# Optimization experiments

Hardware: AMD Instinct MI355X
Metric: run time of the kernel (lower is better)

Reference implementation:

```python
import jax, jax.numpy as jnp
import numpy as np

WINDOW = 4  # window_size
H = 8       # n_heads


def setup_inputs() -> dict:
    key = jax.random.key(0)
    ks = jax.random.split(key, 12)
    B, C, T = 4, 512, 1024
    d = C // H
    x = jax.random.normal(ks[0], (B, C, T), dtype=jnp.float32)
    mask = jnp.ones((B, 1, 1, T), dtype=jnp.int32)
    s = 0.02
    Wq = jax.random.normal(ks[1], (C, C), dtype=jnp.float32) * s
    Wk = jax.random.normal(ks[2], (C, C), dtype=jnp.float32) * s
    Wv = jax.random.normal(ks[3], (C, C), dtype=jnp.float32) * s
    Wo = jax.random.normal(ks[4], (C, C), dtype=jnp.float32) * s
    bq = jnp.zeros((C,), jnp.float32)
    bk = jnp.zeros((C,), jnp.float32)
    bv = jnp.zeros((C,), jnp.float32)
    bo = jnp.zeros((C,), jnp.float32)
    rel_std = d ** (-0.5)
    emb_rel_k = jax.random.normal(ks[5], (1, 2 * WINDOW + 1, d), dtype=jnp.float32) * rel_std
    emb_rel_v = jax.random.normal(ks[6], (1, 2 * WINDOW + 1, d), dtype=jnp.float32) * rel_std
    return {"x": x, "mask": mask, "Wq": Wq, "bq": bq, "Wk": Wk, "bk": bk,
            "Wv": Wv, "bv": bv, "Wo": Wo, "bo": bo,
            "emb_rel_k": emb_rel_k, "emb_rel_v": emb_rel_v}


def _slice_rel_emb(emb, T, pad_len, start, end):
    # F.pad(emb, [0,0,pad,pad,0,0]) then [:, start:end] -> [1, 2T-1, d]
    p = jnp.pad(emb, ((0, 0), (pad_len, pad_len), (0, 0)))
    return p[:, start:end]


def reference(x, mask, Wq, bq, Wk, bk, Wv, bv, Wo, bo, emb_rel_k, emb_rel_v):
    B, C, T = x.shape
    d = C // H
    scale = jnp.asarray(np.sqrt(d), x.dtype)

    def proj(Wm, bm):
        return jnp.einsum('oc,bct->bot', Wm, x) + bm[None, :, None]

    def to_heads(t):  # [B,C,T] -> [B,H,T,d]
        return t.reshape(B, H, d, T).transpose(0, 1, 3, 2)

    query = to_heads(proj(Wq, bq))
    key_ = to_heads(proj(Wk, bk))
    value = to_heads(proj(Wv, bv))

    score = jnp.einsum('bhtd,bhsd->bhts', query, key_) / scale

    pad_len = max(0, T - (WINDOW + 1))
    start = max(0, WINDOW + 1 - T)
    end = start + 2 * T - 1

    k_emb = _slice_rel_emb(emb_rel_k, T, pad_len, start, end)  # [1, 2T-1, d]
    rel = jnp.einsum('bhtd,rd->bhtr', query, k_emb[0])          # [B,H,T,2T-1]
    # skew trick: relative -> absolute
    rel = jnp.pad(rel, ((0, 0), (0, 0), (0, 0), (0, 1))).reshape(B, H, 2 * T * T)
    rel = jnp.pad(rel, ((0, 0), (0, 0), (0, T - 1))).reshape(B, H, T + 1, 2 * T - 1)
    score_loc = rel[:, :, :T, T - 1:] / scale
    score = score + score_loc

    score = jnp.where(mask == 0, jnp.asarray(-10000.0, score.dtype), score)
    p_attn = jax.nn.softmax(score, axis=-1)  # dropout=0 (eval)

    output = jnp.einsum('bhts,bhsd->bhtd', p_attn, value)

    # inverse skew: absolute -> relative weights [B,H,T,2T-1]
    pw = jnp.pad(p_attn, ((0, 0), (0, 0), (0, 0), (0, T - 1))).reshape(B, H, T * (2 * T - 1))
    pw = jnp.pad(pw, ((0, 0), (0, 0), (T, 0))).reshape(B, H, T, 2 * T)[:, :, :, 1:]
    v_emb = _slice_rel_emb(emb_rel_v, T, pad_len, start, end)  # [1, 2T-1, d]
    output = output + jnp.einsum('bhtr,rd->bhtd', pw, v_emb[0])

    out = output.transpose(0, 1, 3, 2).reshape(B, C, T)
    return jnp.einsum('oc,bct->bot', Wo, out) + bo[None, :, None]
```

## Files before the change

### kernel.cpp

```cpp
#include <hip/hip_runtime.h>

typedef unsigned short u16;
typedef unsigned int u32;
using f32x4 = __attribute__((ext_vector_type(4))) float;
using s16x8 = __attribute__((ext_vector_type(8))) short;
using u16x4 = __attribute__((ext_vector_type(4))) unsigned short;
using u16x8 = __attribute__((ext_vector_type(8))) unsigned short;

#define GLOAD_LDS16(g, s)                                     \
  __builtin_amdgcn_global_load_lds(                           \
      (const __attribute__((address_space(1))) void*)(g),     \
      (__attribute__((address_space(3))) void*)(s), 16, 0, 0)

namespace {

constexpr int T = 1024;
constexpr int C = 512;
constexpr float QSCALE = 0.125f * 1.4426950408889634f;
constexpr float MASKED = -14427.0f;
constexpr float DEFER_THR = 11.0f;

__device__ inline u16 f2bf(float f) {
  u32 u = __builtin_bit_cast(u32, f);
  u32 r = (u + 0x7fffu + ((u >> 16) & 1u)) >> 16;
  return (u16)r;
}
__device__ inline float bf2f(u16 v) {
  return __builtin_bit_cast(float, (u32)v << 16);
}
__device__ inline f32x4 mfma16(s16x8 a, s16x8 b, f32x4 c) {
  return __builtin_amdgcn_mfma_f32_16x16x32_bf16(a, b, c, 0, 0, 0);
}
__device__ inline u32 cvtpk(float lo, float hi) {
  u32 r;
  asm("v_cvt_pk_bf16_f32 %0, %1, %2" : "=v"(r) : "v"(lo), "v"(hi));
  return r;
}

__global__ __launch_bounds__(256) void convert_all(
    const float* __restrict__ x, const float* __restrict__ Wq,
    const float* __restrict__ Wk, const float* __restrict__ Wv,
    const float* __restrict__ Wo, u16* __restrict__ xb, u16* __restrict__ Wqb,
    u16* __restrict__ Wkb, u16* __restrict__ Wvb, u16* __restrict__ Wob) {
  const int tid = threadIdx.x;
  const int bid = blockIdx.x;
  const float* src;
  u16* dst;
  size_t off;
  if (bid < 2048) {
    src = x; dst = xb;
    off = ((size_t)bid * 256 + tid) * 4;
  } else {
    const int j = bid - 2048;
    const int w = j >> 8;
    src = w == 0 ? Wq : w == 1 ? Wk : w == 2 ? Wv : Wo;
    dst = w == 0 ? Wqb : w == 1 ? Wkb : w == 2 ? Wvb : Wob;
    off = (((size_t)(j & 255)) * 256 + tid) * 4;
  }
  const float4 v = *reinterpret_cast<const float4*>(src + off);
  u16x4 o;
  o[0] = f2bf(v.x); o[1] = f2bf(v.y); o[2] = f2bf(v.z); o[3] = f2bf(v.w);
  *reinterpret_cast<u16x4*>(dst + off) = o;
}

__global__ __launch_bounds__(256) void qkv_gemm(
    const u16* __restrict__ xb, const u16* __restrict__ Wqb,
    const u16* __restrict__ Wkb, const u16* __restrict__ Wvb,
    const float* __restrict__ bq, const float* __restrict__ bk,
    const float* __restrict__ bv, u16* __restrict__ qb, u16* __restrict__ kswz,
    u16* __restrict__ vswz) {
  __shared__ u16 Bs[2][128 * 32];
  __shared__ float sbias[64];
  const int tid = threadIdx.x;
  const int z = blockIdx.z;
  const int b = z / 3, wsel = z - 3 * b;
  const u16* W = wsel == 0 ? Wqb : wsel == 1 ? Wkb : Wvb;
  const float* bias = wsel == 0 ? bq : wsel == 1 ? bk : bv;
  const int o0 = blockIdx.y * 64;
  const int t0 = blockIdx.x * 128;
  if (tid < 16)
    *reinterpret_cast<float4*>(&sbias[tid * 4]) =
        *reinterpret_cast<const float4*>(&bias[o0 + tid * 4]);

  const int l = tid & 63, wid = tid >> 6;
  const int wm = wid >> 1, wn = wid & 1;
  const int lr = l & 15, lg = l >> 4;

  const int cpair = tid & 15, tgrp = tid >> 4;
  const u16* xrow =
      xb + ((size_t)(b * C) + 2 * cpair) * T + t0 + 8 * tgrp;

  const u16* Arow0 = W + (size_t)(o0 + 32 * wm + lr) * C + 8 * lg;
  const u16* Arow1 = Arow0 + 16 * C;

  f32x4 acc[2][4] = {};

  auto stage = [&](int kk, int buf) {
    const u16* p = xrow + (size_t)kk * 32 * T;
    const u16x8 v0 = *reinterpret_cast<const u16x8*>(p);
    const u16x8 v1 = *reinterpret_cast<const u16x8*>(p + T);
    char* base = (char*)&Bs[buf][0];
#pragma unroll
    for (int j = 0; j < 8; ++j) {
      const int t = 8 * tgrp + j;
      const u32 w2 = (u32)v0[j] | ((u32)v1[j] << 16);
      *(u32*)(base + ((t * 64 + 4 * cpair) ^ ((t & 3) << 4))) = w2;
    }
  };

  s16x8 a0 = *reinterpret_cast<const s16x8*>(Arow0);
  s16x8 a1 = *reinterpret_cast<const s16x8*>(Arow1);
  stage(0, 0);
  __syncthreads();

  for (int kk = 0; kk < 16; ++kk) {
    s16x8 an0, an1;
    if (kk < 15) {
      an0 = *reinterpret_cast<const s16x8*>(Arow0 + (kk + 1) * 32);
      an1 = *reinterpret_cast<const s16x8*>(Arow1 + (kk + 1) * 32);
      stage(kk + 1, (kk + 1) & 1);
    }
    const char* rb = (const char*)&Bs[kk & 1][0];
#pragma unroll
    for (int nf = 0; nf < 4; ++nf) {
      const int t = 64 * wn + 16 * nf + lr;
      const s16x8 bfrag = *reinterpret_cast<const s16x8*>(
          rb + ((t * 64 + 16 * lg) ^ ((t & 3) << 4)));
      acc[0][nf] = mfma16(a0, bfrag, acc[0][nf]);
      acc[1][nf] = mfma16(a1, bfrag, acc[1][nf]);
    }
    __syncthreads();
    if (kk < 15) { a0 = an0; a1 = an1; }
  }

  const int h = o0 >> 6;
  const size_t bh = (size_t)(b * 8 + h);
  if (wsel == 0) {
#pragma unroll
    for (int m = 0; m < 2; ++m) {
      const int ob = 32 * wm + 16 * m + 4 * lg;
#pragma unroll
      for (int nf = 0; nf < 4; ++nf) {
        const int t = t0 + 64 * wn + 16 * nf + lr;
        u16x4 pk;
#pragma unroll
        for (int r = 0; r < 4; ++r)
          pk[r] = f2bf((acc[m][nf][r] + sbias[ob + r]) * QSCALE);
        *reinterpret_cast<u16x4*>(&qb[(bh * T + t) * 64 + ob]) = pk;
      }
    }
  } else if (wsel == 1) {
    char* kbase = (char*)kswz;
#pragma unroll
    for (int m = 0; m < 2; ++m) {
      const int ob = 32 * wm + 16 * m + 4 * lg;
#pragma unroll
      for (int nf = 0; nf < 4; ++nf) {
        const int t = t0 + 64 * wn + 16 * nf + lr;
        const int tile = t >> 6, row = t & 63;
        u16x4 pk;
#pragma unroll
        for (int r = 0; r < 4; ++r) pk[r] = f2bf(acc[m][nf][r] + sbias[ob + r]);
        const int off = (row * 128 + 2 * ob) ^ ((row & 7) << 4);
        *(u16x4*)(kbase + (bh * 16 + tile) * 8192 + off) = pk;
      }
    }
  } else {
    char* vbase = (char*)vswz;
#pragma unroll
    for (int m = 0; m < 2; ++m) {
      const int ob = 32 * wm + 16 * m + 4 * lg;
#pragma unroll
      for (int nf = 0; nf < 4; ++nf) {
        const int t = t0 + 64 * wn + 16 * nf + lr;
        const int tile = t >> 6, col2 = 2 * (t & 63);
#pragma unroll
        for (int r = 0; r < 4; ++r) {
          const int dd = ob + r;
          const int off = (dd * 128 + col2) ^ ((dd & 7) << 4);
          *(u16*)(vbase + (bh * 16 + tile) * 8192 + off) =
              f2bf(acc[m][nf][r] + sbias[dd]);
        }
      }
    }
  }
}

__global__ __launch_bounds__(512) void attn_swapped(
    const u16* __restrict__ qb, const u16* __restrict__ kswz,
    const u16* __restrict__ vswz, const int* __restrict__ gmask,
    const float* __restrict__ ek, const float* __restrict__ ev,
    u16* __restrict__ op0, u16* __restrict__ op1, float2* __restrict__ mlb) {
  __shared__ u16 Kbuf[2][4096];
  __shared__ u16 Vbuf[2][4096];
  __shared__ char QsPd[16384];
  __shared__ float rkk[128][12];
  __shared__ float eks[9][64];
  __shared__ float evs[9][64];
  __shared__ u16 zerobuf[16];
  __shared__ int tflag[16];

  const int z = blockIdx.z;
  const int b = z >> 1, shalf = z & 1;
  const int h = blockIdx.y, tc = blockIdx.x * 128;
  const int tid = threadIdx.x;
  const int l = tid & 63, wid = tid >> 6;
  const int lr = l & 15, lg = l >> 4;

  const size_t bh = (size_t)(b * 8 + h);
  const u16* qrow = qb + (bh * T + tc) * 64;
  const u16* kimg0 = kswz + bh * 65536;
  const u16* vimg0 = vswz + bh * 65536;

  {
    char* qs = QsPd;
#pragma unroll
    for (int rep = 0; rep < 2; ++rep) {
      const int idx = rep * 512 + tid;
      const int t = idx >> 3, slot = idx & 7;
      const u16x8 v =
          *reinterpret_cast<const u16x8*>(&qrow[(size_t)t * 64 + 8 * slot]);
      *(u16x8*)(qs + ((t * 128 + 16 * slot) ^ ((t & 7) << 4))) = v;
    }
  }
  if (tid < 144) {
    reinterpret_cast<float4*>(&eks[0][0])[tid] =
        reinterpret_cast<const float4*>(ek)[tid];
    reinterpret_cast<float4*>(&evs[0][0])[tid] =
        reinterpret_cast<const float4*>(ev)[tid];
  }
  if (tid < 16) { tflag[tid] = 1; zerobuf[tid] = 0; }
  __syncthreads();

  if (tid < 256) {
    const int4 mm = reinterpret_cast<const int4*>(gmask + b * T)[tid];
    if (!(mm.x && mm.y && mm.z && mm.w)) tflag[tid >> 4] = 0;
  }

  auto stage_tile = [&](int st_abs, int buf) {
    const u16* ki = kimg0 + (size_t)st_abs * 4096;
    const u16* vi = vimg0 + (size_t)st_abs * 4096;
    GLOAD_LDS16(ki + wid * 512 + l * 8, &Kbuf[buf][wid * 512]);
    GLOAD_LDS16(vi + wid * 512 + l * 8, &Vbuf[buf][wid * 512]);
  };
  const int st0 = shalf * 8;
  stage_tile(st0, 0);

  {
    const char* qs = QsPd;
    for (int task = tid; task < 1152; task += 512) {
      const int r = task / 9, w = task - 9 * r;
      float s = 0.f;
      const float* er = &eks[w][0];
#pragma unroll 8
      for (int dd = 0; dd < 64; ++dd) {
        const u16 qv = *(const u16*)(qs + ((r * 128 + 2 * dd) ^ ((r & 7) << 4)));
        s += bf2f(qv) * er[dd];
      }
      rkk[r][w] = s;
    }
  }

  const int tA = 16 * wid + lr;
  s16x8 aq0, aq1;
  {
    const char* qs = QsPd;
    aq0 = *reinterpret_cast<const s16x8*>(
        qs + ((tA * 128 + 16 * lg) ^ ((tA & 7) << 4)));
    aq1 = *reinterpret_cast<const s16x8*>(
        qs + ((tA * 128 + 16 * (lg + 4)) ^ ((tA & 7) << 4)));
  }
  __syncthreads();

  u16* Pd = (u16*)(QsPd + wid * 512);

  s16x8 evA[4];
#pragma unroll
  for (int nf = 0; nf < 4; ++nf) {
    const int dd = 16 * nf + lr;
#pragma unroll
    for (int e = 0; e < 8; ++e) {
      float v = 0.f;
      if (lg == 0) v = evs[e][dd];
      else if (lg == 1 && e == 0) v = evs[8][dd];
      evA[nf][e] = (short)f2bf(v);
    }
  }

  float m = -1e30f, lsum = 0.f;
  f32x4 Oa[4] = {};
  const int tbw = tc + 16 * wid;
  const int qg = tbw + lr;

  int cur = 0;
  for (int i = 0; i < 8; ++i) {
    const int st = st0 + i;
    const int s0 = st * 64;
    if (i < 7) stage_tile(st + 1, cur ^ 1);

    f32x4 St[4] = {};
    const char* ksb = (const char*)&Kbuf[cur][0];
#pragma unroll
    for (int nf = 0; nf < 4; ++nf) {
      const int srow = 16 * nf + lr;
      const int swz = (srow & 7) << 4;
      const s16x8 bk0 = *reinterpret_cast<const s16x8*>(
          ksb + ((srow * 128 + 16 * lg) ^ swz));
      const s16x8 bk1 = *reinterpret_cast<const s16x8*>(
          ksb + ((srow * 128 + 16 * (lg + 4)) ^ swz));
      St[nf] = mfma16(bk0, aq0, St[nf]);
      St[nf] = mfma16(bk1, aq1, St[nf]);
    }

    const bool diagw = (s0 <= tbw + 19) && (s0 + 63 >= tbw - 4);

    if (diagw) {
#pragma unroll
      for (int nf = 0; nf < 4; ++nf)
#pragma unroll
        for (int r = 0; r < 4; ++r) {
          const int sd = (s0 + 16 * nf + 4 * lg + r) - qg;
          if (sd >= -4 && sd <= 4) St[nf][r] += rkk[16 * wid + lr][sd + 4];
        }
    }
    if (!tflag[st]) {
#pragma unroll
      for (int nf = 0; nf < 4; ++nf)
#pragma unroll
        for (int r = 0; r < 4; ++r) {
          if (gmask[b * T + s0 + 16 * nf + 4 * lg + r] == 0)
            St[nf][r] = MASKED;
        }
    }

    float rm;
    {
      float m0 = fmaxf(fmaxf(St[0][0], St[0][1]), fmaxf(St[0][2], St[0][3]));
      float m1 = fmaxf(fmaxf(St[1][0], St[1][1]), fmaxf(St[1][2], St[1][3]));
      float m2 = fmaxf(fmaxf(St[2][0], St[2][1]), fmaxf(St[2][2], St[2][3]));
      float m3 = fmaxf(fmaxf(St[3][0], St[3][1]), fmaxf(St[3][2], St[3][3]));
      rm = fmaxf(fmaxf(m0, m1), fmaxf(m2, m3));
      rm = fmaxf(rm, __shfl_xor(rm, 16));
      rm = fmaxf(rm, __shfl_xor(rm, 32));
    }
    if (!__all(rm - m <= DEFER_THR)) {
      const float mn = fmaxf(m, rm);
      const float corr = exp2f(m - mn);
#pragma unroll
      for (int nf = 0; nf < 4; ++nf) {
        Oa[nf][0] *= corr; Oa[nf][1] *= corr;
        Oa[nf][2] *= corr; Oa[nf][3] *= corr;
      }
      lsum *= corr;
      m = mn;
    }
    float rs = 0.f;
#pragma unroll
    for (int nf = 0; nf < 4; ++nf)
#pragma unroll
      for (int r = 0; r < 4; ++r) {
        const float p = exp2f(St[nf][r] - m);
        St[nf][r] = p;
        rs += p;
      }
    rs += __shfl_xor(rs, 16);
    rs += __shfl_xor(rs, 32);
    lsum += rs;

    u32 wpk[4][2];
#pragma unroll
    for (int nf = 0; nf < 4; ++nf) {
      wpk[nf][0] = cvtpk(St[nf][0], St[nf][1]);
      wpk[nf][1] = cvtpk(St[nf][2], St[nf][3]);
    }

    if (diagw) {
      u32* pz = (u32*)Pd;
      pz[l] = 0; pz[l + 64] = 0;
#pragma unroll
      for (int nf = 0; nf < 4; ++nf)
#pragma unroll
        for (int r = 0; r < 4; ++r) {
          const int sd = (s0 + 16 * nf + 4 * lg + r) - qg;
          if (sd >= -4 && sd <= 4) Pd[lr * 16 + sd + 4] = f2bf(St[nf][r]);
        }
    }

    const int srcLo = lr + ((lg & 1) << 5);
    const int srcHi = srcLo + 16;
    const bool hiSel = (lg >> 1) != 0;
    union { u32 u[4]; s16x8 v; } pa0, pa1;
    {
      const u32 a0_ = __shfl((int)wpk[0][0], srcLo), b0_ = __shfl((int)wpk[1][0], srcLo);
      const u32 a1_ = __shfl((int)wpk[0][1], srcLo), b1_ = __shfl((int)wpk[1][1], srcLo);
      const u32 a2_ = __shfl((int)wpk[0][0], srcHi), b2_ = __shfl((int)wpk[1][0], srcHi);
      const u32 a3_ = __shfl((int)wpk[0][1], srcHi), b3_ = __shfl((int)wpk[1][1], srcHi);
      pa0.u[0] = hiSel ? b0_ : a0_; pa0.u[1] = hiSel ? b1_ : a1_;
      pa0.u[2] = hiSel ? b2_ : a2_; pa0.u[3] = hiSel ? b3_ : a3_;
    }
    {
      const u32 a0_ = __shfl((int)wpk[2][0], srcLo), b0_ = __shfl((int)wpk[3][0], srcLo);
      const u32 a1_ = __shfl((int)wpk[2][1], srcLo), b1_ = __shfl((int)wpk[3][1], srcLo);
      const u32 a2_ = __shfl((int)wpk[2][0], srcHi), b2_ = __shfl((int)wpk[3][0], srcHi);
      const u32 a3_ = __shfl((int)wpk[2][1], srcHi), b3_ = __shfl((int)wpk[3][1], srcHi);
      pa1.u[0] = hiSel ? b0_ : a0_; pa1.u[1] = hiSel ? b1_ : a1_;
      pa1.u[2] = hiSel ? b2_ : a2_; pa1.u[3] = hiSel ? b3_ : a3_;
    }

    const char* vsb = (const char*)&Vbuf[cur][0];
#pragma unroll
    for (int nf = 0; nf < 4; ++nf) {
      const int dd = 16 * nf + lr;
      const int swz = (dd & 7) << 4;
      const s16x8 bv0 = *reinterpret_cast<const s16x8*>(
          vsb + ((dd * 128 + 16 * lg) ^ swz));
      const s16x8 bv1 = *reinterpret_cast<const s16x8*>(
          vsb + ((dd * 128 + 16 * (lg + 4)) ^ swz));
      Oa[nf] = mfma16(bv0, pa0.v, Oa[nf]);
      Oa[nf] = mfma16(bv1, pa1.v, Oa[nf]);
    }

    if (diagw) {
      const u16* pdsrc = (lg < 2) ? &Pd[lr * 16 + 8 * lg] : &zerobuf[0];
      const s16x8 pd = *reinterpret_cast<const s16x8*>(pdsrc);
#pragma unroll
      for (int nf = 0; nf < 4; ++nf) Oa[nf] = mfma16(evA[nf], pd, Oa[nf]);
    }

    __syncthreads();
    cur ^= 1;
  }

  u16* op = shalf ? op1 : op0;
#pragma unroll
  for (int nf = 0; nf < 4; ++nf) {
    u16x4 pk;
#pragma unroll
    for (int r = 0; r < 4; ++r) pk[r] = f2bf(Oa[nf][r]);
    *reinterpret_cast<u16x4*>(
        &op[(bh * T + qg) * 64 + 16 * nf + 4 * lg]) = pk;
  }
  if (lg == 0) {
    float2 v;
    v.x = m;
    v.y = lsum;
    mlb[(size_t)shalf * 32768 + bh * T + qg] = v;
  }
}

__global__ __launch_bounds__(256) void merge_halves(
    const u16* __restrict__ op0, const u16* __restrict__ op1,
    const float2* __restrict__ mlb, u16* __restrict__ attb) {
  const int tid = threadIdx.x;
  const int row = blockIdx.x * 16 + (tid >> 4);
  const int dd = (tid & 15) * 4;
  const float2 ml0 = mlb[row];
  const float2 ml1 = mlb[32768 + row];
  const float mm = fmaxf(ml0.x, ml1.x);
  const float a0 = exp2f(ml0.x - mm), a1 = exp2f(ml1.x - mm);
  const float inv = 1.0f / (a0 * ml0.y + a1 * ml1.y);
  const u16x4 v0 = *reinterpret_cast<const u16x4*>(&op0[(size_t)row * 64 + dd]);
  const u16x4 v1 = *reinterpret_cast<const u16x4*>(&op1[(size_t)row * 64 + dd]);
  u16x4 o;
#pragma unroll
  for (int j = 0; j < 4; ++j)
    o[j] = f2bf((bf2f(v0[j]) * a0 + bf2f(v1[j]) * a1) * inv);
  *reinterpret_cast<u16x4*>(&attb[(size_t)row * 64 + dd]) = o;
}

__global__ __launch_bounds__(256) void out_gemm(
    const u16* __restrict__ Wob, const float* __restrict__ bo,
    const u16* __restrict__ attb, float* __restrict__ out) {
  __shared__ u16 Bs[2][128 * 32];
  __shared__ float sbias[64];
  const int tid = threadIdx.x;
  const int b = blockIdx.z;
  const int o0 = blockIdx.y * 64;
  const int t0 = blockIdx.x * 128;
  if (tid < 16)
    *reinterpret_cast<float4*>(&sbias[tid * 4]) =
        *reinterpret_cast<const float4*>(&bo[o0 + tid * 4]);

  const int l = tid & 63, wid = tid >> 6;
  const int wm = wid >> 1, wn = wid & 1;
  const int lr = l & 15, lg = l >> 4;

  const int slot = tid & 3, trow = tid >> 2;
  const u16* Arow0 = Wob + (size_t)(o0 + 32 * wm + lr) * C + 8 * lg;
  const u16* Arow1 = Arow0 + 16 * C;

  f32x4 acc[2][4] = {};

  auto stage = [&](int kk, int buf) {
    const int c0 = kk * 32;
    const int h = c0 >> 6, dd0 = c0 & 63;
    char* base = (char*)&Bs[buf][0];
#pragma unroll
    for (int rep = 0; rep < 2; ++rep) {
      const int t = rep * 64 + trow;
      const u16x8 v = *reinterpret_cast<const u16x8*>(
          &attb[((size_t)((b * 8 + h) * T) + t0 + t) * 64 + dd0 + 8 * slot]);
      *(u16x8*)(base + ((t * 64 + 16 * slot) ^ ((t & 3) << 4))) = v;
    }
  };

  s16x8 a0 = *reinterpret_cast<const s16x8*>(Arow0);
  s16x8 a1 = *reinterpret_cast<const s16x8*>(Arow1);
  stage(0, 0);
  __syncthreads();

  for (int kk = 0; kk < 16; ++kk) {
    s16x8 an0, an1;
    if (kk < 15) {
      an0 = *reinterpret_cast<const s16x8*>(Arow0 + (kk + 1) * 32);
      an1 = *reinterpret_cast<const s16x8*>(Arow1 + (kk + 1) * 32);
      stage(kk + 1, (kk + 1) & 1);
    }
    const char* rb = (const char*)&Bs[kk & 1][0];
#pragma unroll
    for (int nf = 0; nf < 4; ++nf) {
      const int t = 64 * wn + 16 * nf + lr;
      const s16x8 bfrag = *reinterpret_cast<const s16x8*>(
          rb + ((t * 64 + 16 * lg) ^ ((t & 3) << 4)));
      acc[0][nf] = mfma16(a0, bfrag, acc[0][nf]);
      acc[1][nf] = mfma16(a1, bfrag, acc[1][nf]);
    }
    __syncthreads();
    if (kk < 15) { a0 = an0; a1 = an1; }
  }

#pragma unroll
  for (int m = 0; m < 2; ++m) {
    const int ol = 32 * wm + 16 * m + 4 * lg;
#pragma unroll
    for (int nf = 0; nf < 4; ++nf) {
      const int t = t0 + 64 * wn + 16 * nf + lr;
#pragma unroll
      for (int r = 0; r < 4; ++r)
        out[((size_t)(b * C) + o0 + ol + r) * T + t] =
            acc[m][nf][r] + sbias[ol + r];
    }
  }
}

}

extern "C" void kernel_launch(void* const* d_in, const int* in_sizes, int n_in,
                              void* d_out, int out_size, void* d_ws,
                              size_t ws_size, hipStream_t stream) {
  const float* x    = (const float*)d_in[0];
  const int*   mask = (const int*)d_in[1];
  const float* Wq   = (const float*)d_in[2];
  const float* bq   = (const float*)d_in[3];
  const float* Wk   = (const float*)d_in[4];
  const float* bk   = (const float*)d_in[5];
  const float* Wv   = (const float*)d_in[6];
  const float* bv   = (const float*)d_in[7];
  const float* Wo   = (const float*)d_in[8];
  const float* bo   = (const float*)d_in[9];
  const float* ek   = (const float*)d_in[10];
  const float* ev   = (const float*)d_in[11];
  float* out = (float*)d_out;

  char* ws = (char*)d_ws;
  u16* xb   = (u16*)(ws);
  u16* Wqb  = (u16*)(ws + 4194304);
  u16* Wkb  = (u16*)(ws + 4718592);
  u16* Wvb  = (u16*)(ws + 5242880);
  u16* Wob  = (u16*)(ws + 5767168);
  u16* qb   = (u16*)(ws + 6291456);
  u16* kswz = (u16*)(ws + 10485760);
  u16* vswz = (u16*)(ws + 14680064);
  u16* attb = (u16*)(ws + 18874368);
  u16* op0  = xb;
  u16* op1  = (u16*)(ws + 23068672);
  float2* mlb = (float2*)(ws + 27262976);

  convert_all<<<dim3(3072), dim3(256), 0, stream>>>(x, Wq, Wk, Wv, Wo, xb, Wqb,
                                                    Wkb, Wvb, Wob);
  qkv_gemm<<<dim3(8, 8, 12), dim3(256), 0, stream>>>(xb, Wqb, Wkb, Wvb, bq, bk,
                                                     bv, qb, kswz, vswz);
  attn_swapped<<<dim3(8, 8, 8), dim3(512), 0, stream>>>(
      qb, kswz, vswz, mask, ek, ev, op0, op1, mlb);
  merge_halves<<<dim3(2048), dim3(256), 0, stream>>>(op0, op1, mlb, attb);
  out_gemm<<<dim3(8, 8, 4), dim3(256), 0, stream>>>(Wob, bo, attb, out);
}
```

Baseline: 89.11 us.

## Fuse bf16 conversion into GEMMs and split attention keys into thirds

Drops the separate convert_all kernel: both the QKV and output GEMMs now load fp32 x and weights directly and pack them to bf16 in registers with v_cvt_pk_bf16_f32. The attention kernel splits the key range into three chunks instead of two, which raises the block count, and a three-way merge kernel combines them. It also loads Q fragments straight from global memory and computes the relative-key dot products with a 4-lane shuffle reduction, which frees the Q staging buffer in LDS. In exchange the GEMMs read twice the bytes per operand and convert the same data again in every block that uses it, and the merge reads one more partial buffer.

```diff
diff --git a/kernel.cpp b/kernel.cpp
--- a/kernel.cpp
+++ b/kernel.cpp
@@ -36,36 +36,20 @@
   asm("v_cvt_pk_bf16_f32 %0, %1, %2" : "=v"(r) : "v"(lo), "v"(hi));
   return r;
 }
-
-__global__ __launch_bounds__(256) void convert_all(
+__device__ inline s16x8 ldfrag_f32(const float* p) {
+  const float4 f0 = *reinterpret_cast<const float4*>(p);
+  const float4 f1 = *reinterpret_cast<const float4*>(p + 4);
+  union { u32 u[4]; s16x8 v; } r;
+  r.u[0] = cvtpk(f0.x, f0.y);
+  r.u[1] = cvtpk(f0.z, f0.w);
+  r.u[2] = cvtpk(f1.x, f1.y);
+  r.u[3] = cvtpk(f1.z, f1.w);
+  return r.v;
+}
+
+__global__ __launch_bounds__(256) void qkv_gemm(
     const float* __restrict__ x, const float* __restrict__ Wq,
     const float* __restrict__ Wk, const float* __restrict__ Wv,
-    const float* __restrict__ Wo, u16* __restrict__ xb, u16* __restrict__ Wqb,
-    u16* __restrict__ Wkb, u16* __restrict__ Wvb, u16* __restrict__ Wob) {
-  const int tid = threadIdx.x;
-  const int bid = blockIdx.x;
-  const float* src;
-  u16* dst;
-  size_t off;
-  if (bid < 2048) {
-    src = x; dst = xb;
-    off = ((size_t)bid * 256 + tid) * 4;
-  } else {
-    const int j = bid - 2048;
-    const int w = j >> 8;
-    src = w == 0 ? Wq : w == 1 ? Wk : w == 2 ? Wv : Wo;
-    dst = w == 0 ? Wqb : w == 1 ? Wkb : w == 2 ? Wvb : Wob;
-    off = (((size_t)(j & 255)) * 256 + tid) * 4;
-  }
-  const float4 v = *reinterpret_cast<const float4*>(src + off);
-  u16x4 o;
-  o[0] = f2bf(v.x); o[1] = f2bf(v.y); o[2] = f2bf(v.z); o[3] = f2bf(v.w);
-  *reinterpret_cast<u16x4*>(dst + off) = o;
-}
-
-__global__ __launch_bounds__(256) void qkv_gemm(
-    const u16* __restrict__ xb, const u16* __restrict__ Wqb,
-    const u16* __restrict__ Wkb, const u16* __restrict__ Wvb,
     const float* __restrict__ bq, const float* __restrict__ bk,
     const float* __restrict__ bv, u16* __restrict__ qb, u16* __restrict__ kswz,
     u16* __restrict__ vswz) {
@@ -74,7 +58,7 @@
   const int tid = threadIdx.x;
   const int z = blockIdx.z;
   const int b = z / 3, wsel = z - 3 * b;
-  const u16* W = wsel == 0 ? Wqb : wsel == 1 ? Wkb : Wvb;
+  const float* W = wsel == 0 ? Wq : wsel == 1 ? Wk : Wv;
   const float* bias = wsel == 0 ? bq : wsel == 1 ? bk : bv;
   const int o0 = blockIdx.y * 64;
   const int t0 = blockIdx.x * 128;
@@ -87,37 +71,40 @@
   const int lr = l & 15, lg = l >> 4;
 
   const int cpair = tid & 15, tgrp = tid >> 4;
-  const u16* xrow =
-      xb + ((size_t)(b * C) + 2 * cpair) * T + t0 + 8 * tgrp;
-
-  const u16* Arow0 = W + (size_t)(o0 + 32 * wm + lr) * C + 8 * lg;
-  const u16* Arow1 = Arow0 + 16 * C;
+  const float* xrow = x + ((size_t)(b * C) + 2 * cpair) * T + t0 + 8 * tgrp;
+
+  const float* Arow0 = W + (size_t)(o0 + 32 * wm + lr) * C + 8 * lg;
+  const float* Arow1 = Arow0 + 16 * C;
 
   f32x4 acc[2][4] = {};
 
   auto stage = [&](int kk, int buf) {
-    const u16* p = xrow + (size_t)kk * 32 * T;
-    const u16x8 v0 = *reinterpret_cast<const u16x8*>(p);
-    const u16x8 v1 = *reinterpret_cast<const u16x8*>(p + T);
+    const float* p = xrow + (size_t)kk * 32 * T;
+    const float4 e0 = *reinterpret_cast<const float4*>(p);
+    const float4 e1 = *reinterpret_cast<const float4*>(p + 4);
+    const float4 o0_ = *reinterpret_cast<const float4*>(p + T);
+    const float4 o1_ = *reinterpret_cast<const float4*>(p + T + 4);
+    const float ev_[8] = {e0.x, e0.y, e0.z, e0.w, e1.x, e1.y, e1.z, e1.w};
+    const float od_[8] = {o0_.x, o0_.y, o0_.z, o0_.w, o1_.x, o1_.y, o1_.z, o1_.w};
     char* base = (char*)&Bs[buf][0];
 #pragma unroll
     for (int j = 0; j < 8; ++j) {
       const int t = 8 * tgrp + j;
-      const u32 w2 = (u32)v0[j] | ((u32)v1[j] << 16);
+      const u32 w2 = cvtpk(ev_[j], od_[j]);
       *(u32*)(base + ((t * 64 + 4 * cpair) ^ ((t & 3) << 4))) = w2;
     }
   };
 
-  s16x8 a0 = *reinterpret_cast<const s16x8*>(Arow0);
-  s16x8 a1 = *reinterpret_cast<const s16x8*>(Arow1);
+  s16x8 a0 = ldfrag_f32(Arow0);
+  s16x8 a1 = ldfrag_f32(Arow1);
   stage(0, 0);
   __syncthreads();
 
   for (int kk = 0; kk < 16; ++kk) {
     s16x8 an0, an1;
     if (kk < 15) {
-      an0 = *reinterpret_cast<const s16x8*>(Arow0 + (kk + 1) * 32);
-      an1 = *reinterpret_cast<const s16x8*>(Arow1 + (kk + 1) * 32);
+      an0 = ldfrag_f32(Arow0 + (kk + 1) * 32);
+      an1 = ldfrag_f32(Arow1 + (kk + 1) * 32);
       stage(kk + 1, (kk + 1) & 1);
     }
     const char* rb = (const char*)&Bs[kk & 1][0];
@@ -190,10 +177,11 @@
     const u16* __restrict__ qb, const u16* __restrict__ kswz,
     const u16* __restrict__ vswz, const int* __restrict__ gmask,
     const float* __restrict__ ek, const float* __restrict__ ev,
-    u16* __restrict__ op0, u16* __restrict__ op1, float2* __restrict__ mlb) {
+    u16* __restrict__ op0, u16* __restrict__ op1, u16* __restrict__ op2,
+    float2* __restrict__ mlb) {
   __shared__ u16 Kbuf[2][4096];
   __shared__ u16 Vbuf[2][4096];
-  __shared__ char QsPd[16384];
+  __shared__ u16 Pdiag[8][256];
   __shared__ float rkk[128][12];
   __shared__ float eks[9][64];
   __shared__ float evs[9][64];
@@ -201,28 +189,19 @@
   __shared__ int tflag[16];
 
   const int z = blockIdx.z;
-  const int b = z >> 1, shalf = z & 1;
+  const int b = z / 3, third = z - 3 * b;
   const int h = blockIdx.y, tc = blockIdx.x * 128;
   const int tid = threadIdx.x;
   const int l = tid & 63, wid = tid >> 6;
   const int lr = l & 15, lg = l >> 4;
+  const int stS = (third == 0) ? 0 : (third == 1) ? 6 : 11;
+  const int stE = (third == 0) ? 6 : (third == 1) ? 11 : 16;
 
   const size_t bh = (size_t)(b * 8 + h);
-  const u16* qrow = qb + (bh * T + tc) * 64;
+  const u16* qbh = qb + bh * T * 64;
   const u16* kimg0 = kswz + bh * 65536;
   const u16* vimg0 = vswz + bh * 65536;
 
-  {
-    char* qs = QsPd;
-#pragma unroll
-    for (int rep = 0; rep < 2; ++rep) {
-      const int idx = rep * 512 + tid;
-      const int t = idx >> 3, slot = idx & 7;
-      const u16x8 v =
-          *reinterpret_cast<const u16x8*>(&qrow[(size_t)t * 64 + 8 * slot]);
-      *(u16x8*)(qs + ((t * 128 + 16 * slot) ^ ((t & 7) << 4))) = v;
-    }
-  }
   if (tid < 144) {
     reinterpret_cast<float4*>(&eks[0][0])[tid] =
         reinterpret_cast<const float4*>(ek)[tid];
@@ -231,11 +210,6 @@
   }
   if (tid < 16) { tflag[tid] = 1; zerobuf[tid] = 0; }
   __syncthreads();
-
-  if (tid < 256) {
-    const int4 mm = reinterpret_cast<const int4*>(gmask + b * T)[tid];
-    if (!(mm.x && mm.y && mm.z && mm.w)) tflag[tid >> 4] = 0;
-  }
 
   auto stage_tile = [&](int st_abs, int buf) {
     const u16* ki = kimg0 + (size_t)st_abs * 4096;
@@ -243,36 +217,52 @@
     GLOAD_LDS16(ki + wid * 512 + l * 8, &Kbuf[buf][wid * 512]);
     GLOAD_LDS16(vi + wid * 512 + l * 8, &Vbuf[buf][wid * 512]);
   };
-  const int st0 = shalf * 8;
-  stage_tile(st0, 0);
+  stage_tile(stS, 0);
+
+  if (tid < 256) {
+    const int4 mm = reinterpret_cast<const int4*>(gmask + b * T)[tid];
+    if (!(mm.x && mm.y && mm.z && mm.w)) tflag[tid >> 4] = 0;
+  }
 
   {
-    const char* qs = QsPd;
-    for (int task = tid; task < 1152; task += 512) {
-      const int r = task / 9, w = task - 9 * r;
+    const int r = tid >> 2, sub = tid & 3;
+    const u16* qp = qbh + (size_t)(tc + r) * 64 + sub * 16;
+    const u16x8 q0 = *reinterpret_cast<const u16x8*>(qp);
+    const u16x8 q1 = *reinterpret_cast<const u16x8*>(qp + 8);
+    float qf[16];
+#pragma unroll
+    for (int j = 0; j < 8; ++j) {
+      qf[j] = bf2f(q0[j]);
+      qf[j + 8] = bf2f(q1[j]);
+    }
+    float part[9];
+#pragma unroll
+    for (int w = 0; w < 9; ++w) {
       float s = 0.f;
-      const float* er = &eks[w][0];
-#pragma unroll 8
-      for (int dd = 0; dd < 64; ++dd) {
-        const u16 qv = *(const u16*)(qs + ((r * 128 + 2 * dd) ^ ((r & 7) << 4)));
-        s += bf2f(qv) * er[dd];
-      }
-      rkk[r][w] = s;
-    }
-  }
-
-  const int tA = 16 * wid + lr;
+      const float* er = &eks[w][sub * 16];
+#pragma unroll
+      for (int d = 0; d < 16; ++d) s += qf[d] * er[d];
+      part[w] = s;
+    }
+#pragma unroll
+    for (int w = 0; w < 9; ++w) {
+      part[w] += __shfl_xor(part[w], 1);
+      part[w] += __shfl_xor(part[w], 2);
+    }
+    if (sub == 0) {
+#pragma unroll
+      for (int w = 0; w < 9; ++w) rkk[r][w] = part[w];
+    }
+  }
+
+  const int tbw = tc + 16 * wid;
+  const int qg = tbw + lr;
   s16x8 aq0, aq1;
   {
-    const char* qs = QsPd;
-    aq0 = *reinterpret_cast<const s16x8*>(
-        qs + ((tA * 128 + 16 * lg) ^ ((tA & 7) << 4)));
-    aq1 = *reinterpret_cast<const s16x8*>(
-        qs + ((tA * 128 + 16 * (lg + 4)) ^ ((tA & 7) << 4)));
-  }
-  __syncthreads();
-
-  u16* Pd = (u16*)(QsPd + wid * 512);
+    const u16* qgp = qbh + (size_t)qg * 64;
+    aq0 = *reinterpret_cast<const s16x8*>(qgp + 8 * lg);
+    aq1 = *reinterpret_cast<const s16x8*>(qgp + 32 + 8 * lg);
+  }
 
   s16x8 evA[4];
 #pragma unroll
@@ -289,14 +279,14 @@
 
   float m = -1e30f, lsum = 0.f;
   f32x4 Oa[4] = {};
-  const int tbw = tc + 16 * wid;
-  const int qg = tbw + lr;
+  u16* Pd = &Pdiag[wid][0];
+
+  __syncthreads();
 
   int cur = 0;
-  for (int i = 0; i < 8; ++i) {
-    const int st = st0 + i;
+  for (int st = stS; st < stE; ++st) {
     const int s0 = st * 64;
-    if (i < 7) stage_tile(st + 1, cur ^ 1);
+    if (st + 1 < stE) stage_tile(st + 1, cur ^ 1);
 
     f32x4 St[4] = {};
     const char* ksb = (const char*)&Kbuf[cur][0];
@@ -431,7 +421,7 @@
     cur ^= 1;
   }
 
-  u16* op = shalf ? op1 : op0;
+  u16* op = (third == 0) ? op0 : (third == 1) ? op1 : op2;
 #pragma unroll
   for (int nf = 0; nf < 4; ++nf) {
     u16x4 pk;
@@ -444,32 +434,36 @@
     float2 v;
     v.x = m;
     v.y = lsum;
-    mlb[(size_t)shalf * 32768 + bh * T + qg] = v;
-  }
-}
-
-__global__ __launch_bounds__(256) void merge_halves(
+    mlb[(size_t)third * 32768 + bh * T + qg] = v;
+  }
+}
+
+__global__ __launch_bounds__(256) void merge_thirds(
     const u16* __restrict__ op0, const u16* __restrict__ op1,
-    const float2* __restrict__ mlb, u16* __restrict__ attb) {
+    const u16* __restrict__ op2, const float2* __restrict__ mlb,
+    u16* __restrict__ attb) {
   const int tid = threadIdx.x;
   const int row = blockIdx.x * 16 + (tid >> 4);
   const int dd = (tid & 15) * 4;
   const float2 ml0 = mlb[row];
   const float2 ml1 = mlb[32768 + row];
-  const float mm = fmaxf(ml0.x, ml1.x);
-  const float a0 = exp2f(ml0.x - mm), a1 = exp2f(ml1.x - mm);
-  const float inv = 1.0f / (a0 * ml0.y + a1 * ml1.y);
+  const float2 ml2 = mlb[65536 + row];
+  const float mm = fmaxf(fmaxf(ml0.x, ml1.x), ml2.x);
+  const float a0 = exp2f(ml0.x - mm), a1 = exp2f(ml1.x - mm),
+              a2 = exp2f(ml2.x - mm);
+  const float inv = 1.0f / (a0 * ml0.y + a1 * ml1.y + a2 * ml2.y);
   const u16x4 v0 = *reinterpret_cast<const u16x4*>(&op0[(size_t)row * 64 + dd]);
   const u16x4 v1 = *reinterpret_cast<const u16x4*>(&op1[(size_t)row * 64 + dd]);
+  const u16x4 v2 = *reinterpret_cast<const u16x4*>(&op2[(size_t)row * 64 + dd]);
   u16x4 o;
 #pragma unroll
   for (int j = 0; j < 4; ++j)
-    o[j] = f2bf((bf2f(v0[j]) * a0 + bf2f(v1[j]) * a1) * inv);
+    o[j] = f2bf((bf2f(v0[j]) * a0 + bf2f(v1[j]) * a1 + bf2f(v2[j]) * a2) * inv);
   *reinterpret_cast<u16x4*>(&attb[(size_t)row * 64 + dd]) = o;
 }
 
 __global__ __launch_bounds__(256) void out_gemm(
-    const u16* __restrict__ Wob, const float* __restrict__ bo,
+    const float* __restrict__ Wo, const float* __restrict__ bo,
     const u16* __restrict__ attb, float* __restrict__ out) {
   __shared__ u16 Bs[2][128 * 32];
   __shared__ float sbias[64];
@@ -486,8 +480,8 @@
   const int lr = l & 15, lg = l >> 4;
 
   const int slot = tid & 3, trow = tid >> 2;
-  const u16* Arow0 = Wob + (size_t)(o0 + 32 * wm + lr) * C + 8 * lg;
-  const u16* Arow1 = Arow0 + 16 * C;
+  const float* Arow0 = Wo + (size_t)(o0 + 32 * wm + lr) * C + 8 * lg;
+  const float* Arow1 = Arow0 + 16 * C;
 
   f32x4 acc[2][4] = {};
 
@@ -504,16 +498,16 @@
     }
   };
 
-  s16x8 a0 = *reinterpret_cast<const s16x8*>(Arow0);
-  s16x8 a1 = *reinterpret_cast<const s16x8*>(Arow1);
+  s16x8 a0 = ldfrag_f32(Arow0);
+  s16x8 a1 = ldfrag_f32(Arow1);
   stage(0, 0);
   __syncthreads();
 
   for (int kk = 0; kk < 16; ++kk) {
     s16x8 an0, an1;
     if (kk < 15) {
-      an0 = *reinterpret_cast<const s16x8*>(Arow0 + (kk + 1) * 32);
-      an1 = *reinterpret_cast<const s16x8*>(Arow1 + (kk + 1) * 32);
+      an0 = ldfrag_f32(Arow0 + (kk + 1) * 32);
+      an1 = ldfrag_f32(Arow1 + (kk + 1) * 32);
       stage(kk + 1, (kk + 1) & 1);
     }
     const char* rb = (const char*)&Bs[kk & 1][0];
@@ -563,25 +557,19 @@
   float* out = (float*)d_out;
 
   char* ws = (char*)d_ws;
-  u16* xb   = (u16*)(ws);
-  u16* Wqb  = (u16*)(ws + 4194304);
-  u16* Wkb  = (u16*)(ws + 4718592);
-  u16* Wvb  = (u16*)(ws + 5242880);
-  u16* Wob  = (u16*)(ws + 5767168);
-  u16* qb   = (u16*)(ws + 6291456);
-  u16* kswz = (u16*)(ws + 10485760);
-  u16* vswz = (u16*)(ws + 14680064);
-  u16* attb = (u16*)(ws + 18874368);
-  u16* op0  = xb;
-  u16* op1  = (u16*)(ws + 23068672);
-  float2* mlb = (float2*)(ws + 27262976);
-
-  convert_all<<<dim3(3072), dim3(256), 0, stream>>>(x, Wq, Wk, Wv, Wo, xb, Wqb,
-                                                    Wkb, Wvb, Wob);
-  qkv_gemm<<<dim3(8, 8, 12), dim3(256), 0, stream>>>(xb, Wqb, Wkb, Wvb, bq, bk,
-                                                     bv, qb, kswz, vswz);
-  attn_swapped<<<dim3(8, 8, 8), dim3(512), 0, stream>>>(
-      qb, kswz, vswz, mask, ek, ev, op0, op1, mlb);
-  merge_halves<<<dim3(2048), dim3(256), 0, stream>>>(op0, op1, mlb, attb);
-  out_gemm<<<dim3(8, 8, 4), dim3(256), 0, stream>>>(Wob, bo, attb, out);
-}
+  u16* qb   = (u16*)(ws);
+  u16* kswz = (u16*)(ws + 4194304);
+  u16* vswz = (u16*)(ws + 8388608);
+  u16* op0  = (u16*)(ws + 12582912);
+  u16* op1  = (u16*)(ws + 16777216);
+  u16* op2  = (u16*)(ws + 20971520);
+  float2* mlb = (float2*)(ws + 25165824);
+  u16* attb = op0;
+
+  qkv_gemm<<<dim3(8, 8, 12), dim3(256), 0, stream>>>(x, Wq, Wk, Wv, bq, bk, bv,
+                                                     qb, kswz, vswz);
+  attn_swapped<<<dim3(8, 8, 12), dim3(512), 0, stream>>>(
+      qb, kswz, vswz, mask, ek, ev, op0, op1, op2, mlb);
+  merge_thirds<<<dim3(2048), dim3(256), 0, stream>>>(op0, op1, op2, mlb, attb);
+  out_gemm<<<dim3(8, 8, 4), dim3(256), 0, stream>>>(Wo, bo, attb, out);
+}
```

After: 113.1 us. 27.0% more time.

## Process two key tiles per iteration and load Q fragments directly from global

Applied to the files above, without the earlier changes.

The attention loop now stages and consumes pairs of 64-key K/V tiles per iteration, halving the number of barriers and loop trips while interleaving independent MFMA chains for the two score tiles. Q is no longer staged through shared memory: MFMA fragments are read straight from global, and the relative-key bias dot products are computed by four lanes per row with shuffle reductions. The costs are doubled K/V LDS buffers and more live registers, which may lower occupancy.

```diff
diff --git a/kernel.cpp b/kernel.cpp
--- a/kernel.cpp
+++ b/kernel.cpp
@@ -191,9 +191,9 @@
     const u16* __restrict__ vswz, const int* __restrict__ gmask,
     const float* __restrict__ ek, const float* __restrict__ ev,
     u16* __restrict__ op0, u16* __restrict__ op1, float2* __restrict__ mlb) {
-  __shared__ u16 Kbuf[2][4096];
-  __shared__ u16 Vbuf[2][4096];
-  __shared__ char QsPd[16384];
+  __shared__ u16 Kbuf[2][8192];
+  __shared__ u16 Vbuf[2][8192];
+  __shared__ u16 Pdiag[8][256];
   __shared__ float rkk[128][12];
   __shared__ float eks[9][64];
   __shared__ float evs[9][64];
@@ -208,21 +208,10 @@
   const int lr = l & 15, lg = l >> 4;
 
   const size_t bh = (size_t)(b * 8 + h);
-  const u16* qrow = qb + (bh * T + tc) * 64;
+  const u16* qbh = qb + bh * T * 64;
   const u16* kimg0 = kswz + bh * 65536;
   const u16* vimg0 = vswz + bh * 65536;
 
-  {
-    char* qs = QsPd;
-#pragma unroll
-    for (int rep = 0; rep < 2; ++rep) {
-      const int idx = rep * 512 + tid;
-      const int t = idx >> 3, slot = idx & 7;
-      const u16x8 v =
-          *reinterpret_cast<const u16x8*>(&qrow[(size_t)t * 64 + 8 * slot]);
-      *(u16x8*)(qs + ((t * 128 + 16 * slot) ^ ((t & 7) << 4))) = v;
-    }
-  }
   if (tid < 144) {
     reinterpret_cast<float4*>(&eks[0][0])[tid] =
         reinterpret_cast<const float4*>(ek)[tid];
@@ -232,47 +221,63 @@
   if (tid < 16) { tflag[tid] = 1; zerobuf[tid] = 0; }
   __syncthreads();
 
+  auto stage_pair = [&](int stp, int buf) {
+    const u16* ki = kimg0 + (size_t)stp * 4096;
+    const u16* vi = vimg0 + (size_t)stp * 4096;
+#pragma unroll
+    for (int j = 0; j < 2; ++j) {
+      const int seg = wid + 8 * j;
+      GLOAD_LDS16(ki + seg * 512 + l * 8, &Kbuf[buf][seg * 512]);
+      GLOAD_LDS16(vi + seg * 512 + l * 8, &Vbuf[buf][seg * 512]);
+    }
+  };
+  const int st0 = shalf * 8;
+  stage_pair(st0, 0);
+
   if (tid < 256) {
     const int4 mm = reinterpret_cast<const int4*>(gmask + b * T)[tid];
     if (!(mm.x && mm.y && mm.z && mm.w)) tflag[tid >> 4] = 0;
   }
 
-  auto stage_tile = [&](int st_abs, int buf) {
-    const u16* ki = kimg0 + (size_t)st_abs * 4096;
-    const u16* vi = vimg0 + (size_t)st_abs * 4096;
-    GLOAD_LDS16(ki + wid * 512 + l * 8, &Kbuf[buf][wid * 512]);
-    GLOAD_LDS16(vi + wid * 512 + l * 8, &Vbuf[buf][wid * 512]);
-  };
-  const int st0 = shalf * 8;
-  stage_tile(st0, 0);
-
   {
-    const char* qs = QsPd;
-    for (int task = tid; task < 1152; task += 512) {
-      const int r = task / 9, w = task - 9 * r;
+    const int r = tid >> 2, sub = tid & 3;
+    const u16* qp = qbh + (size_t)(tc + r) * 64 + sub * 16;
+    const u16x8 q0 = *reinterpret_cast<const u16x8*>(qp);
+    const u16x8 q1 = *reinterpret_cast<const u16x8*>(qp + 8);
+    float qf[16];
+#pragma unroll
+    for (int j = 0; j < 8; ++j) {
+      qf[j] = bf2f(q0[j]);
+      qf[j + 8] = bf2f(q1[j]);
+    }
+    float part[9];
+#pragma unroll
+    for (int w = 0; w < 9; ++w) {
       float s = 0.f;
-      const float* er = &eks[w][0];
-#pragma unroll 8
-      for (int dd = 0; dd < 64; ++dd) {
-        const u16 qv = *(const u16*)(qs + ((r * 128 + 2 * dd) ^ ((r & 7) << 4)));
-        s += bf2f(qv) * er[dd];
-      }
-      rkk[r][w] = s;
-    }
-  }
-
-  const int tA = 16 * wid + lr;
+      const float* er = &eks[w][sub * 16];
+#pragma unroll
+      for (int d = 0; d < 16; ++d) s += qf[d] * er[d];
+      part[w] = s;
+    }
+#pragma unroll
+    for (int w = 0; w < 9; ++w) {
+      part[w] += __shfl_xor(part[w], 1);
+      part[w] += __shfl_xor(part[w], 2);
+    }
+    if (sub == 0) {
+#pragma unroll
+      for (int w = 0; w < 9; ++w) rkk[r][w] = part[w];
+    }
+  }
+
+  const int tbw = tc + 16 * wid;
+  const int qg = tbw + lr;
   s16x8 aq0, aq1;
   {
-    const char* qs = QsPd;
-    aq0 = *reinterpret_cast<const s16x8*>(
-        qs + ((tA * 128 + 16 * lg) ^ ((tA & 7) << 4)));
-    aq1 = *reinterpret_cast<const s16x8*>(
-        qs + ((tA * 128 + 16 * (lg + 4)) ^ ((tA & 7) << 4)));
-  }
-  __syncthreads();
-
-  u16* Pd = (u16*)(QsPd + wid * 512);
+    const u16* qgp = qbh + (size_t)qg * 64;
+    aq0 = *reinterpret_cast<const s16x8*>(qgp + 8 * lg);
+    aq1 = *reinterpret_cast<const s16x8*>(qgp + 32 + 8 * lg);
+  }
 
   s16x8 evA[4];
 #pragma unroll
@@ -289,103 +294,17 @@
 
   float m = -1e30f, lsum = 0.f;
   f32x4 Oa[4] = {};
-  const int tbw = tc + 16 * wid;
-  const int qg = tbw + lr;
-
-  int cur = 0;
-  for (int i = 0; i < 8; ++i) {
-    const int st = st0 + i;
-    const int s0 = st * 64;
-    if (i < 7) stage_tile(st + 1, cur ^ 1);
-
-    f32x4 St[4] = {};
-    const char* ksb = (const char*)&Kbuf[cur][0];
-#pragma unroll
-    for (int nf = 0; nf < 4; ++nf) {
-      const int srow = 16 * nf + lr;
-      const int swz = (srow & 7) << 4;
-      const s16x8 bk0 = *reinterpret_cast<const s16x8*>(
-          ksb + ((srow * 128 + 16 * lg) ^ swz));
-      const s16x8 bk1 = *reinterpret_cast<const s16x8*>(
-          ksb + ((srow * 128 + 16 * (lg + 4)) ^ swz));
-      St[nf] = mfma16(bk0, aq0, St[nf]);
-      St[nf] = mfma16(bk1, aq1, St[nf]);
-    }
-
-    const bool diagw = (s0 <= tbw + 19) && (s0 + 63 >= tbw - 4);
-
-    if (diagw) {
-#pragma unroll
-      for (int nf = 0; nf < 4; ++nf)
-#pragma unroll
-        for (int r = 0; r < 4; ++r) {
-          const int sd = (s0 + 16 * nf + 4 * lg + r) - qg;
-          if (sd >= -4 && sd <= 4) St[nf][r] += rkk[16 * wid + lr][sd + 4];
-        }
-    }
-    if (!tflag[st]) {
-#pragma unroll
-      for (int nf = 0; nf < 4; ++nf)
-#pragma unroll
-        for (int r = 0; r < 4; ++r) {
-          if (gmask[b * T + s0 + 16 * nf + 4 * lg + r] == 0)
-            St[nf][r] = MASKED;
-        }
-    }
-
-    float rm;
-    {
-      float m0 = fmaxf(fmaxf(St[0][0], St[0][1]), fmaxf(St[0][2], St[0][3]));
-      float m1 = fmaxf(fmaxf(St[1][0], St[1][1]), fmaxf(St[1][2], St[1][3]));
-      float m2 = fmaxf(fmaxf(St[2][0], St[2][1]), fmaxf(St[2][2], St[2][3]));
-      float m3 = fmaxf(fmaxf(St[3][0], St[3][1]), fmaxf(St[3][2], St[3][3]));
-      rm = fmaxf(fmaxf(m0, m1), fmaxf(m2, m3));
-      rm = fmaxf(rm, __shfl_xor(rm, 16));
-      rm = fmaxf(rm, __shfl_xor(rm, 32));
-    }
-    if (!__all(rm - m <= DEFER_THR)) {
-      const float mn = fmaxf(m, rm);
-      const float corr = exp2f(m - mn);
-#pragma unroll
-      for (int nf = 0; nf < 4; ++nf) {
-        Oa[nf][0] *= corr; Oa[nf][1] *= corr;
-        Oa[nf][2] *= corr; Oa[nf][3] *= corr;
-      }
-      lsum *= corr;
-      m = mn;
-    }
-    float rs = 0.f;
-#pragma unroll
-    for (int nf = 0; nf < 4; ++nf)
-#pragma unroll
-      for (int r = 0; r < 4; ++r) {
-        const float p = exp2f(St[nf][r] - m);
-        St[nf][r] = p;
-        rs += p;
-      }
-    rs += __shfl_xor(rs, 16);
-    rs += __shfl_xor(rs, 32);
-    lsum += rs;
-
+  u16* Pd = &Pdiag[wid][0];
+
+  __syncthreads();
+
+  auto redist = [&](const f32x4* St, s16x8& pv0, s16x8& pv1) {
     u32 wpk[4][2];
 #pragma unroll
     for (int nf = 0; nf < 4; ++nf) {
       wpk[nf][0] = cvtpk(St[nf][0], St[nf][1]);
       wpk[nf][1] = cvtpk(St[nf][2], St[nf][3]);
     }
-
-    if (diagw) {
-      u32* pz = (u32*)Pd;
-      pz[l] = 0; pz[l + 64] = 0;
-#pragma unroll
-      for (int nf = 0; nf < 4; ++nf)
-#pragma unroll
-        for (int r = 0; r < 4; ++r) {
-          const int sd = (s0 + 16 * nf + 4 * lg + r) - qg;
-          if (sd >= -4 && sd <= 4) Pd[lr * 16 + sd + 4] = f2bf(St[nf][r]);
-        }
-    }
-
     const int srcLo = lr + ((lg & 1) << 5);
     const int srcHi = srcLo + 16;
     const bool hiSel = (lg >> 1) != 0;
@@ -406,21 +325,168 @@
       pa1.u[0] = hiSel ? b0_ : a0_; pa1.u[1] = hiSel ? b1_ : a1_;
       pa1.u[2] = hiSel ? b2_ : a2_; pa1.u[3] = hiSel ? b3_ : a3_;
     }
+    pv0 = pa0.v;
+    pv1 = pa1.v;
+  };
+
+  int cur = 0;
+  for (int ii = 0; ii < 4; ++ii) {
+    const int stp = st0 + 2 * ii;
+    const int s0 = stp * 64, s1 = s0 + 64;
+    if (ii < 3) stage_pair(stp + 2, cur ^ 1);
+
+    f32x4 StA[4] = {}, StB[4] = {};
+    const char* ksb = (const char*)&Kbuf[cur][0];
+#pragma unroll
+    for (int nf = 0; nf < 4; ++nf) {
+      const int srow = 16 * nf + lr;
+      const int swz = (srow & 7) << 4;
+      const int o0_ = (srow * 128 + 16 * lg) ^ swz;
+      const int o1_ = (srow * 128 + 16 * (lg + 4)) ^ swz;
+      const s16x8 ka0 = *reinterpret_cast<const s16x8*>(ksb + o0_);
+      const s16x8 ka1 = *reinterpret_cast<const s16x8*>(ksb + o1_);
+      const s16x8 kb0 = *reinterpret_cast<const s16x8*>(ksb + 8192 + o0_);
+      const s16x8 kb1 = *reinterpret_cast<const s16x8*>(ksb + 8192 + o1_);
+      StA[nf] = mfma16(ka0, aq0, StA[nf]);
+      StB[nf] = mfma16(kb0, aq0, StB[nf]);
+      StA[nf] = mfma16(ka1, aq1, StA[nf]);
+      StB[nf] = mfma16(kb1, aq1, StB[nf]);
+    }
+
+    const bool diagA = (s0 <= tbw + 19) && (s0 + 63 >= tbw - 4);
+    const bool diagB = (s1 <= tbw + 19) && (s1 + 63 >= tbw - 4);
+
+    if (diagA) {
+#pragma unroll
+      for (int nf = 0; nf < 4; ++nf)
+#pragma unroll
+        for (int r = 0; r < 4; ++r) {
+          const int sd = (s0 + 16 * nf + 4 * lg + r) - qg;
+          if (sd >= -4 && sd <= 4) StA[nf][r] += rkk[16 * wid + lr][sd + 4];
+        }
+    }
+    if (diagB) {
+#pragma unroll
+      for (int nf = 0; nf < 4; ++nf)
+#pragma unroll
+        for (int r = 0; r < 4; ++r) {
+          const int sd = (s1 + 16 * nf + 4 * lg + r) - qg;
+          if (sd >= -4 && sd <= 4) StB[nf][r] += rkk[16 * wid + lr][sd + 4];
+        }
+    }
+    if (!tflag[stp]) {
+#pragma unroll
+      for (int nf = 0; nf < 4; ++nf)
+#pragma unroll
+        for (int r = 0; r < 4; ++r)
+          if (gmask[b * T + s0 + 16 * nf + 4 * lg + r] == 0) StA[nf][r] = MASKED;
+    }
+    if (!tflag[stp + 1]) {
+#pragma unroll
+      for (int nf = 0; nf < 4; ++nf)
+#pragma unroll
+        for (int r = 0; r < 4; ++r)
+          if (gmask[b * T + s1 + 16 * nf + 4 * lg + r] == 0) StB[nf][r] = MASKED;
+    }
+
+    float rm;
+    {
+      float mv = fmaxf(fmaxf(StA[0][0], StA[0][1]), fmaxf(StA[0][2], StA[0][3]));
+#pragma unroll
+      for (int nf = 1; nf < 4; ++nf)
+        mv = fmaxf(mv, fmaxf(fmaxf(StA[nf][0], StA[nf][1]),
+                             fmaxf(StA[nf][2], StA[nf][3])));
+#pragma unroll
+      for (int nf = 0; nf < 4; ++nf)
+        mv = fmaxf(mv, fmaxf(fmaxf(StB[nf][0], StB[nf][1]),
+                             fmaxf(StB[nf][2], StB[nf][3])));
+      rm = mv;
+      rm = fmaxf(rm, __shfl_xor(rm, 16));
+      rm = fmaxf(rm, __shfl_xor(rm, 32));
+    }
+    if (!__all(rm - m <= DEFER_THR)) {
+      const float mn = fmaxf(m, rm);
+      const float corr = exp2f(m - mn);
+#pragma unroll
+      for (int nf = 0; nf < 4; ++nf) {
+        Oa[nf][0] *= corr; Oa[nf][1] *= corr;
+        Oa[nf][2] *= corr; Oa[nf][3] *= corr;
+      }
+      lsum *= corr;
+      m = mn;
+    }
+    float rs = 0.f;
+#pragma unroll
+    for (int nf = 0; nf < 4; ++nf)
+#pragma unroll
+      for (int r = 0; r < 4; ++r) {
+        const float pA = exp2f(StA[nf][r] - m);
+        const float pB = exp2f(StB[nf][r] - m);
+        StA[nf][r] = pA;
+        StB[nf][r] = pB;
+        rs += pA + pB;
+      }
+    rs += __shfl_xor(rs, 16);
+    rs += __shfl_xor(rs, 32);
+    lsum += rs;
+
+    const bool diagP = diagA || diagB;
+    if (diagP) {
+      u32* pz = (u32*)Pd;
+      pz[l] = 0; pz[l + 64] = 0;
+      if (diagA) {
+#pragma unroll
+        for (int nf = 0; nf < 4; ++nf)
+#pragma unroll
+          for (int r = 0; r < 4; ++r) {
+            const int sd = (s0 + 16 * nf + 4 * lg + r) - qg;
+            if (sd >= -4 && sd <= 4) Pd[lr * 16 + sd + 4] = f2bf(StA[nf][r]);
+          }
+      }
+      if (diagB) {
+#pragma unroll
+        for (int nf = 0; nf < 4; ++nf)
+#pragma unroll
+          for (int r = 0; r < 4; ++r) {
+            const int sd = (s1 + 16 * nf + 4 * lg + r) - qg;
+            if (sd >= -4 && sd <= 4) Pd[lr * 16 + sd + 4] = f2bf(StB[nf][r]);
+          }
+      }
+    }
 
     const char* vsb = (const char*)&Vbuf[cur][0];
-#pragma unroll
-    for (int nf = 0; nf < 4; ++nf) {
-      const int dd = 16 * nf + lr;
-      const int swz = (dd & 7) << 4;
-      const s16x8 bv0 = *reinterpret_cast<const s16x8*>(
-          vsb + ((dd * 128 + 16 * lg) ^ swz));
-      const s16x8 bv1 = *reinterpret_cast<const s16x8*>(
-          vsb + ((dd * 128 + 16 * (lg + 4)) ^ swz));
-      Oa[nf] = mfma16(bv0, pa0.v, Oa[nf]);
-      Oa[nf] = mfma16(bv1, pa1.v, Oa[nf]);
-    }
-
-    if (diagw) {
+    {
+      s16x8 pa0, pa1;
+      redist(StA, pa0, pa1);
+#pragma unroll
+      for (int nf = 0; nf < 4; ++nf) {
+        const int dd = 16 * nf + lr;
+        const int swz = (dd & 7) << 4;
+        const s16x8 bv0 = *reinterpret_cast<const s16x8*>(
+            vsb + ((dd * 128 + 16 * lg) ^ swz));
+        const s16x8 bv1 = *reinterpret_cast<const s16x8*>(
+            vsb + ((dd * 128 + 16 * (lg + 4)) ^ swz));
+        Oa[nf] = mfma16(bv0, pa0, Oa[nf]);
+        Oa[nf] = mfma16(bv1, pa1, Oa[nf]);
+      }
+    }
+    {
+      s16x8 pa0, pa1;
+      redist(StB, pa0, pa1);
+#pragma unroll
+      for (int nf = 0; nf < 4; ++nf) {
+        const int dd = 16 * nf + lr;
+        const int swz = (dd & 7) << 4;
+        const s16x8 bv0 = *reinterpret_cast<const s16x8*>(
+            vsb + 8192 + ((dd * 128 + 16 * lg) ^ swz));
+        const s16x8 bv1 = *reinterpret_cast<const s16x8*>(
+            vsb + 8192 + ((dd * 128 + 16 * (lg + 4)) ^ swz));
+        Oa[nf] = mfma16(bv0, pa0, Oa[nf]);
+        Oa[nf] = mfma16(bv1, pa1, Oa[nf]);
+      }
+    }
+
+    if (diagP) {
       const u16* pdsrc = (lg < 2) ? &Pd[lr * 16 + 8 * lg] : &zerobuf[0];
       const s16x8 pd = *reinterpret_cast<const s16x8*>(pdsrc);
 #pragma unroll
```

New measurement: 81.92 us. -8.1%, faster.
